# Kernel optimization log

Hardware: AMD Instinct MI355X
Metric: run time of the kernel (lower is better)

The kernel has to match this reference:

```python
import jax, jax.numpy as jnp
import numpy as np
import math

B, L, D, H, DK, DFF = 4, 1024, 1024, 16, 64, 4096
NUM_BUCKETS, MAX_DIST = 32, 128


def _relative_position_bucket(rel):
    # bidirectional T5 bucketing; rel = memory_pos - context_pos
    nb = NUM_BUCKETS // 2
    n = -rel
    ret = (n < 0).astype(jnp.int32) * nb
    n = jnp.abs(n)
    max_exact = nb // 2
    is_small = n < max_exact
    val_if_large = max_exact + (
        jnp.log(jnp.maximum(n, 1).astype(jnp.float32) / max_exact)
        / math.log(MAX_DIST / max_exact)
        * (nb - max_exact)
    ).astype(jnp.int32)
    val_if_large = jnp.minimum(val_if_large, nb - 1)
    return ret + jnp.where(is_small, n.astype(jnp.int32), val_if_large)


def t5_layernorm(x, w, eps):
    # no mean subtraction, no bias (T5 style)
    var = jnp.mean(jnp.square(x.astype(jnp.float32)), axis=-1, keepdims=True)
    return w * (x / jnp.sqrt(var + eps))


def setup_inputs() -> dict:
    key = jax.random.key(0)
    ks = jax.random.split(key, 12)
    inp = {
        "src": jax.random.normal(ks[0], (B, L, D), dtype=jnp.float32),
        "enc_position": jnp.broadcast_to(jnp.arange(L, dtype=jnp.int32), (B, L)),
        "ln1_w": jnp.ones((D,), jnp.float32),
        "wq": jax.random.normal(ks[1], (H * DK, D), jnp.float32) * (D * DK) ** -0.5,
        "bq": jnp.zeros((H * DK,), jnp.float32),
        "wk": jax.random.normal(ks[2], (H * DK, D), jnp.float32) * D ** -0.5,
        "bk": jnp.zeros((H * DK,), jnp.float32),
        "wv": jax.random.normal(ks[3], (H * DK, D), jnp.float32) * D ** -0.5,
        "bv": jnp.zeros((H * DK,), jnp.float32),
        "fc_w": jax.random.normal(ks[4], (D, H * DK), jnp.float32) * (H * DK) ** -0.5,
        "fc_b": jnp.zeros((D,), jnp.float32),
        "rel_bias": jax.random.normal(ks[5], (NUM_BUCKETS, H), jnp.float32) * 0.02,
        "ln2_w": jnp.ones((D,), jnp.float32),
        "wi": jax.random.normal(ks[6], (DFF, D), jnp.float32) * D ** -0.5,
        "wo": jax.random.normal(ks[7], (D, DFF), jnp.float32) * DFF ** -0.5,
    }
    return inp


def reference(src, enc_position, ln1_w, wq, bq, wk, bk, wv, bv, fc_w, fc_b,
              rel_bias, ln2_w, wi, wo):
    b, l, d = src.shape
    temp = DK ** 0.5

    # --- Multi-head self attention (pre-LN, T5 relative bias) ---
    proj = t5_layernorm(src, ln1_w, 1e-12)
    q = (proj @ wq.T + bq).reshape(b, l, H, DK).transpose(0, 2, 1, 3)  # [b,h,l,dk]
    k = (proj @ wk.T + bk).reshape(b, l, H, DK).transpose(0, 2, 1, 3)
    v = (proj @ wv.T + bv).reshape(b, l, H, DK).transpose(0, 2, 1, 3)

    # relative position bias: [b, h, l_q, l_k]
    rel = enc_position[:, None, :] - enc_position[:, :, None]  # mem - ctx
    bucket = _relative_position_bucket(rel)                    # [b, l, l]
    position_bias = rel_bias[bucket].transpose(0, 3, 1, 2)     # [b, h, l, l]

    scores = jnp.einsum("bhqd,bhkd->bhqk", q / temp, k) + position_bias
    attn = jax.nn.softmax(scores, axis=-1)                     # dropout = eval no-op
    ctx = jnp.einsum("bhqk,bhkd->bhqd", attn, v)
    ctx = ctx.transpose(0, 2, 1, 3).reshape(b, l, H * DK)
    attn_out = ctx @ fc_w.T + fc_b + src                       # residual
    attn_sum = jnp.sum(attn, axis=1)                           # [b, l, l]

    # --- Position-wise FFN (pre-LN, gelu, no biases) ---
    nx = t5_layernorm(attn_out, ln2_w, 1e-6)
    h = jax.nn.gelu(nx @ wi.T, approximate=False)
    out = attn_out + h @ wo.T
    return out, attn_sum, position_bias
```

## Files before the change

### kernel.cpp

```cpp
#include <hip/hip_runtime.h>
#include <hip/hip_bf16.h>
#include <math.h>

typedef __attribute__((ext_vector_type(8))) short short8;
typedef __attribute__((ext_vector_type(4))) float f32x4;
typedef unsigned short u16;

#define L2E 1.44269504088896340736f

__device__ __forceinline__ u16 f2bf(float f) {
  union { float f; unsigned u; } x; x.f = f;
  unsigned r = x.u + 0x7fffu + ((x.u >> 16) & 1u);
  return (u16)(r >> 16);
}

__device__ __forceinline__ void gload16(const void* g, void* l) {
  auto gp = reinterpret_cast<const __attribute__((address_space(1))) void*>(
      reinterpret_cast<uintptr_t>(g));
  auto lp = reinterpret_cast<__attribute__((address_space(3))) void*>(
      reinterpret_cast<uintptr_t>(l));
  __builtin_amdgcn_global_load_lds(gp, lp, 16, 0, 0);
}

__device__ __forceinline__ int xcd_swz(int flat, int nwg) {
  return (flat & 7) * (nwg >> 3) + (flat >> 3);
}

__device__ __forceinline__ int bucket_fn(int rel) {
  int n = -rel;
  int ret = 0;
  if (n < 0) { ret = 16; n = -n; }
  if (n < 8) return ret + n;
  int e = 31 - __clz(n);
  unsigned nn = (unsigned)n * (unsigned)n;
  int f = 2 * e + ((nn >= (1u << (2 * e + 1))) ? 1 : 0) - 6;
  int val = 8 + f;
  if (val > 15) val = 15;
  return ret + val;
}

__global__ __launch_bounds__(256) void prep_ln(
    const float* __restrict__ wq, const float* __restrict__ wk,
    const float* __restrict__ wv, const float* __restrict__ fcw,
    const float* __restrict__ wi, const float* __restrict__ wo,
    const float* __restrict__ bq, const float* __restrict__ bk,
    const float* __restrict__ bv, const float* __restrict__ rel_bias,
    u16* __restrict__ wqb, u16* __restrict__ wkb, u16* __restrict__ wvb,
    u16* __restrict__ fcwb, u16* __restrict__ wib, u16* __restrict__ wob,
    float* __restrict__ fb, float* __restrict__ tab,
    const float* __restrict__ src, const float* __restrict__ ln1_w,
    u16* __restrict__ proj) {
  const int blk = blockIdx.x, t = threadIdx.x;
  if (blk < 12288) {
    const float* s; u16* d; int rel;
    if (blk < 1024)      { s = wq;  d = wqb;  rel = blk; }
    else if (blk < 2048) { s = wk;  d = wkb;  rel = blk - 1024; }
    else if (blk < 3072) { s = wv;  d = wvb;  rel = blk - 2048; }
    else if (blk < 4096) { s = fcw; d = fcwb; rel = blk - 3072; }
    else if (blk < 8192) { s = wi;  d = wib;  rel = blk - 4096; }
    else                 { s = wo;  d = wob;  rel = blk - 8192; }
    const int i = (rel * 256 + t) * 4;
    float4 v = *(const float4*)&s[i];
    d[i + 0] = f2bf(v.x); d[i + 1] = f2bf(v.y);
    d[i + 2] = f2bf(v.z); d[i + 3] = f2bf(v.w);
  } else if (blk < 12300) {
    const int i = (blk - 12288) * 256 + t;
    fb[i] = i < 1024 ? bq[i] : (i < 2048 ? bk[i - 1024] : bv[i - 2048]);
  } else if (blk < 12428) {
    const int idx = (blk - 12300) * 256 + t;
    const int h = idx >> 11;
    const int rel = (idx & 2047) - 1024;
    tab[idx] = rel_bias[bucket_fn(rel) * 16 + h];
  } else {
    const int row = blk - 12428;
    const float4 v = ((const float4*)(src + (size_t)row * 1024))[t];
    float ss = v.x * v.x + v.y * v.y + v.z * v.z + v.w * v.w;
#pragma unroll
    for (int off = 1; off < 64; off <<= 1) ss += __shfl_xor(ss, off, 64);
    __shared__ float red[4];
    if ((t & 63) == 0) red[t >> 6] = ss;
    __syncthreads();
    float tot = red[0] + red[1] + red[2] + red[3];
    float inv = 1.0f / sqrtf(tot * (1.0f / 1024.0f) + 1e-12f);
    const float4 wv = ((const float4*)ln1_w)[t];
    u16* o = proj + (size_t)row * 1024 + t * 4;
    o[0] = f2bf(v.x * inv * wv.x);
    o[1] = f2bf(v.y * inv * wv.y);
    o[2] = f2bf(v.z * inv * wv.z);
    o[3] = f2bf(v.w * inv * wv.w);
  }
}

__global__ __launch_bounds__(256) void t5_ln(const float* __restrict__ x,
                                             const float* __restrict__ wgt,
                                             float eps, u16* __restrict__ out) {
  const int row = blockIdx.x, t = threadIdx.x;
  const float4 v = ((const float4*)(x + (size_t)row * 1024))[t];
  float ss = v.x * v.x + v.y * v.y + v.z * v.z + v.w * v.w;
#pragma unroll
  for (int off = 1; off < 64; off <<= 1) ss += __shfl_xor(ss, off, 64);
  __shared__ float red[4];
  if ((t & 63) == 0) red[t >> 6] = ss;
  __syncthreads();
  float tot = red[0] + red[1] + red[2] + red[3];
  float inv = 1.0f / sqrtf(tot * (1.0f / 1024.0f) + eps);
  const float4 wv = ((const float4*)wgt)[t];
  u16* o = out + (size_t)row * 1024 + t * 4;
  o[0] = f2bf(v.x * inv * wv.x);
  o[1] = f2bf(v.y * inv * wv.y);
  o[2] = f2bf(v.z * inv * wv.z);
  o[3] = f2bf(v.w * inv * wv.w);
}

__global__ __launch_bounds__(256) void transpose_v(const u16* __restrict__ v,
                                                   u16* __restrict__ vt) {
  __shared__ u16 T[64][72];
  const int bh = blockIdx.y;
  const int l0 = blockIdx.x * 64;
  const int t = threadIdx.x;
  const int sr = t >> 3, sc = (t & 7) * 8;
  const u16* vb = v + (size_t)bh * 65536;
  *(short8*)&T[sr][sc]      = *(const short8*)&vb[(size_t)(l0 + sr) * 64 + sc];
  *(short8*)&T[sr + 32][sc] = *(const short8*)&vb[(size_t)(l0 + sr + 32) * 64 + sc];
  __syncthreads();
  u16* vtb = vt + (size_t)bh * 65536;
  short8 o0, o1;
#pragma unroll
  for (int u = 0; u < 8; u++) {
    ((u16*)&o0)[u] = T[sc + u][sr];
    ((u16*)&o1)[u] = T[sc + u][sr + 32];
  }
  *(short8*)&vtb[(size_t)sr * 1024 + l0 + sc]        = o0;
  *(short8*)&vtb[(size_t)(sr + 32) * 1024 + l0 + sc] = o1;
}

template<int MODE>
__global__ __launch_bounds__(256, 3) void gemm_nt(
    const u16* __restrict__ A, const u16* __restrict__ Bw,
    int M, int N, int K,
    const float* __restrict__ bias, const float* __restrict__ res,
    float scale, float* __restrict__ outF, u16* __restrict__ outB) {
  __shared__ u16 As[3][4096];
  __shared__ u16 Bs[3][4096];
  const int t = threadIdx.x;
  const int w = t >> 6, lane = t & 63;
  const int wr = w >> 1, wc = w & 1;
  const int g = lane >> 4, lc = lane & 15;

  const int nwg = gridDim.x * gridDim.y;
  const int flat = xcd_swz(blockIdx.y * gridDim.x + blockIdx.x, nwg);
  const int bx = flat % gridDim.x, by = flat / gridDim.x;
  const int m0 = by * 128, n0 = bx * 128;

  const int srow = w * 16 + (lane >> 2);
  const int sc8  = (lane & 3) ^ ((srow >> 1) & 3);
  const u16* Ag = &A[(size_t)(m0 + srow) * K + sc8 * 8];
  const u16* Bg = &Bw[(size_t)(n0 + srow) * K + sc8 * 8];
  const size_t row64 = (size_t)64 * K;
  const int swz = (lc >> 1) & 3;

  const int NT = K >> 5;
  f32x4 acc[4][4] = {};

  auto stage = [&](int buf, int tt) {
    const int k0 = tt << 5;
    u16* lA = &As[buf][w * 512];
    u16* lB = &Bs[buf][w * 512];
    gload16(Ag + k0, lA);
    gload16(Ag + row64 + k0, lA + 2048);
    gload16(Bg + k0, lB);
    gload16(Bg + row64 + k0, lB + 2048);
  };

  stage(0, 0);
  stage(1, 1);

  for (int tt = 0; tt < NT; tt++) {
    const int cur = tt % 3;
    if (tt < NT - 1) {
      asm volatile("s_waitcnt vmcnt(4)" ::: "memory");
    } else {
      asm volatile("s_waitcnt vmcnt(0)" ::: "memory");
    }
    __builtin_amdgcn_s_barrier();
    if (tt + 2 < NT) stage((tt + 2) % 3, tt + 2);
    short8 af[4], bf[4];
#pragma unroll
    for (int mi = 0; mi < 4; mi++)
      af[mi] = *(short8*)&As[cur][(wr * 64 + mi * 16 + lc) * 32 + (g ^ swz) * 8];
#pragma unroll
    for (int ni = 0; ni < 4; ni++)
      bf[ni] = *(short8*)&Bs[cur][(wc * 64 + ni * 16 + lc) * 32 + (g ^ swz) * 8];
#pragma unroll
    for (int mi = 0; mi < 4; mi++)
#pragma unroll
      for (int ni = 0; ni < 4; ni++)
        acc[mi][ni] = __builtin_amdgcn_mfma_f32_16x16x32_bf16(af[mi], bf[ni], acc[mi][ni], 0, 0, 0);
  }

  u16* Es = &As[0][0];
  __syncthreads();
#pragma unroll
  for (int mi = 0; mi < 4; mi++) {
#pragma unroll
    for (int ni = 0; ni < 4; ni++) {
#pragma unroll
      for (int r = 0; r < 4; r++) {
        const int col = n0 + wc * 64 + ni * 16 + lc;
        float v = acc[mi][ni][r];
        if (MODE == 0) {
          v = (v + bias[col]) * ((col >> 10) == 0 ? scale : 1.0f);
        } else {
          v = 0.5f * v * (1.0f + erff(v * 0.70710678118654752440f));
        }
        Es[wr * 2048 + (g * 4 + r) * 128 + wc * 64 + ni * 16 + lc] = f2bf(v);
      }
    }
    __syncthreads();
    {
      const int rr = t >> 3;
      const int wr2 = rr >> 4, r16 = rr & 15;
      const int cc = (t & 7) * 16;
      short8 o0 = *(short8*)&Es[wr2 * 2048 + r16 * 128 + cc];
      short8 o1 = *(short8*)&Es[wr2 * 2048 + r16 * 128 + cc + 8];
      const int row = m0 + wr2 * 64 + mi * 16 + r16;
      if (MODE == 0) {
        const int col0 = n0 + cc;
        const int which = col0 >> 10, c = col0 & 1023;
        const int hh = c >> 6, dk = c & 63;
        const int b = row >> 10, pos = row & 1023;
        u16* dst = outB + (size_t)which * 4194304 +
                   (((size_t)(b * 16 + hh)) * 1024 + pos) * 64 + dk;
        *(short8*)dst = o0;
        *(short8*)(dst + 8) = o1;
      } else {
        u16* dst = outB + (size_t)row * (size_t)N + n0 + cc;
        *(short8*)dst = o0;
        *(short8*)(dst + 8) = o1;
      }
    }
    __syncthreads();
  }
}

template<int MODE>
__global__ __launch_bounds__(256, 4) void gemm_nt64(
    const u16* __restrict__ A, const u16* __restrict__ Bw,
    int M, int N, int K,
    const float* __restrict__ bias, const float* __restrict__ res,
    float* __restrict__ outF) {
  __shared__ u16 As[3][2048];
  __shared__ u16 Bs[3][4096];
  const int t = threadIdx.x;
  const int w = t >> 6, lane = t & 63;
  const int wr = w >> 1, wc = w & 1;
  const int g = lane >> 4, lc = lane & 15;

  const int nwg = gridDim.x * gridDim.y;
  const int flat = xcd_swz(blockIdx.y * gridDim.x + blockIdx.x, nwg);
  const int bx = flat % gridDim.x, by = flat / gridDim.x;
  const int m0 = by * 64, n0 = bx * 128;

  const int srow = w * 16 + (lane >> 2);
  const int sc8  = (lane & 3) ^ ((srow >> 1) & 3);
  const u16* Ag = &A[(size_t)(m0 + srow) * K + sc8 * 8];
  const u16* Bg = &Bw[(size_t)(n0 + srow) * K + sc8 * 8];
  const size_t row64 = (size_t)64 * K;
  const int swz = (lc >> 1) & 3;

  const int NT = K >> 5;
  f32x4 acc[2][4] = {};

  auto stage = [&](int buf, int tt) {
    const int k0 = tt << 5;
    gload16(Ag + k0, &As[buf][w * 512]);
    gload16(Bg + k0, &Bs[buf][w * 512]);
    gload16(Bg + row64 + k0, &Bs[buf][w * 512 + 2048]);
  };

  stage(0, 0);
  stage(1, 1);

  for (int tt = 0; tt < NT; tt++) {
    const int cur = tt % 3;
    if (tt < NT - 1) {
      asm volatile("s_waitcnt vmcnt(3)" ::: "memory");
    } else {
      asm volatile("s_waitcnt vmcnt(0)" ::: "memory");
    }
    __builtin_amdgcn_s_barrier();
    if (tt + 2 < NT) stage((tt + 2) % 3, tt + 2);
    short8 af[2], bf[4];
#pragma unroll
    for (int mi = 0; mi < 2; mi++)
      af[mi] = *(short8*)&As[cur][(wr * 32 + mi * 16 + lc) * 32 + (g ^ swz) * 8];
#pragma unroll
    for (int ni = 0; ni < 4; ni++)
      bf[ni] = *(short8*)&Bs[cur][(wc * 64 + ni * 16 + lc) * 32 + (g ^ swz) * 8];
#pragma unroll
    for (int mi = 0; mi < 2; mi++)
#pragma unroll
      for (int ni = 0; ni < 4; ni++)
        acc[mi][ni] = __builtin_amdgcn_mfma_f32_16x16x32_bf16(af[mi], bf[ni], acc[mi][ni], 0, 0, 0);
  }

#pragma unroll
  for (int mi = 0; mi < 2; mi++) {
#pragma unroll
    for (int ni = 0; ni < 4; ni++) {
#pragma unroll
      for (int r = 0; r < 4; r++) {
        const int row = m0 + wr * 32 + mi * 16 + g * 4 + r;
        const int col = n0 + wc * 64 + ni * 16 + lc;
        float v = acc[mi][ni][r];
        if (MODE == 1) {
          v += bias[col] + res[(size_t)row * 1024 + col];
        } else {
          v += res[(size_t)row * 1024 + col];
        }
        outF[(size_t)row * 1024 + col] = v;
      }
    }
  }
}

__global__ __launch_bounds__(256, 3) void fc_asum(
    const u16* __restrict__ ctx, const u16* __restrict__ fcw,
    const float* __restrict__ fc_b, const float* __restrict__ src,
    float* __restrict__ attn_out,
    const u16* __restrict__ q, const u16* __restrict__ k,
    const float* __restrict__ tab, const float* __restrict__ ml,
    float* __restrict__ asum) {
  __shared__ char pool[36864];
  const int t = threadIdx.x;
  const int w = t >> 6, lane = t & 63;
  const int g = lane >> 4, lc = lane & 15;

  if (blockIdx.x < 512) {
    u16* As = (u16*)pool;
    u16* Bs = (u16*)(pool + 12288);
    const int wr = w >> 1, wc = w & 1;
    const int flat = xcd_swz(blockIdx.x, 512);
    const int bx = flat & 7, by = flat >> 3;
    const int m0 = by * 64, n0 = bx * 128;
    const int K = 1024;

    const int srow = w * 16 + (lane >> 2);
    const int sc8  = (lane & 3) ^ ((srow >> 1) & 3);
    const u16* Ag = &ctx[(size_t)(m0 + srow) * K + sc8 * 8];
    const u16* Bg = &fcw[(size_t)(n0 + srow) * K + sc8 * 8];
    const size_t row64 = (size_t)64 * K;
    const int swz = (lc >> 1) & 3;

    const int NT = K >> 5;
    f32x4 acc[2][4] = {};

    auto stage = [&](int buf, int tt) {
      const int k0 = tt << 5;
      gload16(Ag + k0, &As[buf * 2048 + w * 512]);
      gload16(Bg + k0, &Bs[buf * 4096 + w * 512]);
      gload16(Bg + row64 + k0, &Bs[buf * 4096 + w * 512 + 2048]);
    };

    stage(0, 0);
    stage(1, 1);

    for (int tt = 0; tt < NT; tt++) {
      const int cur = tt % 3;
      if (tt < NT - 1) {
        asm volatile("s_waitcnt vmcnt(3)" ::: "memory");
      } else {
        asm volatile("s_waitcnt vmcnt(0)" ::: "memory");
      }
      __builtin_amdgcn_s_barrier();
      if (tt + 2 < NT) stage((tt + 2) % 3, tt + 2);
      short8 af[2], bf[4];
#pragma unroll
      for (int mi = 0; mi < 2; mi++)
        af[mi] = *(short8*)&As[cur * 2048 + (wr * 32 + mi * 16 + lc) * 32 + (g ^ swz) * 8];
#pragma unroll
      for (int ni = 0; ni < 4; ni++)
        bf[ni] = *(short8*)&Bs[cur * 4096 + (wc * 64 + ni * 16 + lc) * 32 + (g ^ swz) * 8];
#pragma unroll
      for (int mi = 0; mi < 2; mi++)
#pragma unroll
        for (int ni = 0; ni < 4; ni++)
          acc[mi][ni] = __builtin_amdgcn_mfma_f32_16x16x32_bf16(af[mi], bf[ni], acc[mi][ni], 0, 0, 0);
    }

#pragma unroll
    for (int mi = 0; mi < 2; mi++) {
#pragma unroll
      for (int ni = 0; ni < 4; ni++) {
#pragma unroll
        for (int r = 0; r < 4; r++) {
          const int row = m0 + wr * 32 + mi * 16 + g * 4 + r;
          const int col = n0 + wc * 64 + ni * 16 + lc;
          float v = acc[mi][ni][r] + fc_b[col] + src[(size_t)row * 1024 + col];
          attn_out[(size_t)row * 1024 + col] = v;
        }
      }
    }
  } else {
    u16* Ks = (u16*)pool;
    float* tabs = (float*)(pool + 8192);
    const int flat = xcd_swz(blockIdx.x - 512, 1024);
    const int j0 = (flat % 16) * 64;
    const int i0 = ((flat / 16) % 16) * 64;
    const int b = flat / 256;
    const int sr = t >> 3;
    const int swc = ((t & 7) ^ (sr & 7)) * 8;
    const int sc = (t & 7) * 8;
    const int rx = lc & 7;

    f32x4 acc[4] = {};

    for (int h = 0; h < 16; h++) {
      const int bh = b * 16 + h;
      __syncthreads();
      const u16* kb = k + (size_t)bh * 65536;
      *(short8*)&Ks[sr * 64 + swc]        = *(const short8*)&kb[(size_t)(j0 + sr) * 64 + sc];
      *(short8*)&Ks[(sr + 32) * 64 + swc] = *(const short8*)&kb[(size_t)(j0 + sr + 32) * 64 + sc];
      if (t < 127) tabs[t] = tab[h * 2048 + (j0 - i0 - 63 + t) + 1024] * L2E;
      __syncthreads();
      const u16* qb = q + (size_t)bh * 65536;
      short8 aq0 = *(const short8*)&qb[(size_t)(i0 + w * 16 + lc) * 64 + g * 8];
      short8 aq1 = *(const short8*)&qb[(size_t)(i0 + w * 16 + lc) * 64 + 32 + g * 8];
      f32x4 s[4] = {};
#pragma unroll
      for (int ni = 0; ni < 4; ni++) {
        short8 b0 = *(short8*)&Ks[(ni * 16 + lc) * 64 + (g ^ rx) * 8];
        short8 b1 = *(short8*)&Ks[(ni * 16 + lc) * 64 + ((4 + g) ^ rx) * 8];
        s[ni] = __builtin_amdgcn_mfma_f32_16x16x32_bf16(aq0, b0, s[ni], 0, 0, 0);
        s[ni] = __builtin_amdgcn_mfma_f32_16x16x32_bf16(aq1, b1, s[ni], 0, 0, 0);
      }
      float mm[4], li[4];
#pragma unroll
      for (int r = 0; r < 4; r++) {
        const int i = i0 + w * 16 + g * 4 + r;
        mm[r] = ml[(size_t)bh * 1024 + i];
        li[r] = 1.0f / ml[65536 + (size_t)bh * 1024 + i];
      }
#pragma unroll
      for (int ni = 0; ni < 4; ni++)
#pragma unroll
        for (int r = 0; r < 4; r++) {
          float sv = s[ni][r] + tabs[ni * 16 + lc - w * 16 - g * 4 - r + 63];
          acc[ni][r] += __builtin_amdgcn_exp2f(sv - mm[r]) * li[r];
        }
    }
#pragma unroll
    for (int ni = 0; ni < 4; ni++)
#pragma unroll
      for (int r = 0; r < 4; r++) {
        const int i = i0 + w * 16 + g * 4 + r;
        asum[((size_t)b * 1024 + i) * 1024 + j0 + ni * 16 + lc] = acc[ni][r];
      }
  }
}

__global__ __launch_bounds__(256) void attn_kernel(
    const u16* __restrict__ q, const u16* __restrict__ k,
    const u16* __restrict__ vt, const float* __restrict__ tab,
    u16* __restrict__ ctx, float* __restrict__ ml, float* __restrict__ pb) {
  const int flat = xcd_swz(blockIdx.y * 16 + blockIdx.x, 1024);
  const int bh = flat / 16;
  const int i0 = (flat % 16) * 64;
  const int h = bh & 15, b = bh >> 4;
  const int t = threadIdx.x, w = t >> 6, lane = t & 63;
  const int g = lane >> 4, lc = lane & 15;
  const int sr = t >> 3;
  const int swc = ((t & 7) ^ (sr & 7)) * 8;
  const int sc = (t & 7) * 8;

  __shared__ u16 Ks[2][64][64];
  __shared__ u16 Vts[2][64][64];
  __shared__ u16 P[4][16][64];
  __shared__ float tabs[2048];

  const u16* qb  = q + (size_t)bh * 65536;
  const u16* kb  = k + (size_t)bh * 65536;
  const u16* vtb = vt + (size_t)bh * 65536;

  ((float4*)tabs)[t]       = ((const float4*)(tab + h * 2048))[t];
  ((float4*)tabs)[t + 256] = ((const float4*)(tab + h * 2048))[t + 256];

  const short8 aq0 = *(const short8*)&qb[(size_t)(i0 + w * 16 + lc) * 64 + g * 8];
  const short8 aq1 = *(const short8*)&qb[(size_t)(i0 + w * 16 + lc) * 64 + 32 + g * 8];

  {
    short8 ka = *(const short8*)&kb[(size_t)sr * 64 + sc];
    short8 kc = *(const short8*)&kb[(size_t)(sr + 32) * 64 + sc];
    short8 va = *(const short8*)&vtb[(size_t)sr * 1024 + sc];
    short8 vc = *(const short8*)&vtb[(size_t)(sr + 32) * 1024 + sc];
    *(short8*)&Ks[0][sr][swc]       = ka;
    *(short8*)&Ks[0][sr + 32][swc]  = kc;
    *(short8*)&Vts[0][sr][swc]      = va;
    *(short8*)&Vts[0][sr + 32][swc] = vc;
  }
  __syncthreads();

  const int rx = lc & 7;
  const int ibase = 1024 - i0 - (w * 16 + g * 4) + lc;
  float* pbrow = pb + (size_t)bh * 1048576 + (size_t)i0 * 1024 + t * 4;

  float m_r[4] = {-INFINITY, -INFINITY, -INFINITY, -INFINITY};
  float l_r[4] = {0.f, 0.f, 0.f, 0.f};
  f32x4 cacc[4] = {};

  for (int tt = 0; tt < 16; tt++) {
    const int buf = tt & 1;
    const int j0 = tt * 64;

    short8 nka, nkc, nva, nvc;
    if (tt < 15) {
      const int jn = j0 + 64;
      nka = *(const short8*)&kb[(size_t)(jn + sr) * 64 + sc];
      nkc = *(const short8*)&kb[(size_t)(jn + sr + 32) * 64 + sc];
      nva = *(const short8*)&vtb[(size_t)sr * 1024 + jn + sc];
      nvc = *(const short8*)&vtb[(size_t)(sr + 32) * 1024 + jn + sc];
    }

    f32x4 s[4] = {};
#pragma unroll
    for (int ni = 0; ni < 4; ni++) {
      short8 b0 = *(short8*)&Ks[buf][ni * 16 + lc][(g ^ rx) * 8];
      short8 b1 = *(short8*)&Ks[buf][ni * 16 + lc][((4 + g) ^ rx) * 8];
      s[ni] = __builtin_amdgcn_mfma_f32_16x16x32_bf16(aq0, b0, s[ni], 0, 0, 0);
      s[ni] = __builtin_amdgcn_mfma_f32_16x16x32_bf16(aq1, b1, s[ni], 0, 0, 0);
    }
#pragma unroll
    for (int ni = 0; ni < 4; ni++)
#pragma unroll
      for (int r = 0; r < 4; r++)
        s[ni][r] = fmaf(tabs[ibase + j0 + ni * 16 - r], L2E, s[ni][r]);

#pragma unroll
    for (int r = 0; r < 4; r++) {
      float tm = fmaxf(fmaxf(s[0][r], s[1][r]), fmaxf(s[2][r], s[3][r]));
#pragma unroll
      for (int off = 1; off < 16; off <<= 1) tm = fmaxf(tm, __shfl_xor(tm, off, 64));
      const float mn = fmaxf(m_r[r], tm);
      const float scl = __builtin_amdgcn_exp2f(m_r[r] - mn);
      float rs = 0.f;
#pragma unroll
      for (int ni = 0; ni < 4; ni++) {
        float p = __builtin_amdgcn_exp2f(s[ni][r] - mn);
        s[ni][r] = p;
        rs += p;
      }
#pragma unroll
      for (int off = 1; off < 16; off <<= 1) rs += __shfl_xor(rs, off, 64);
      l_r[r] = l_r[r] * scl + rs;
      m_r[r] = mn;
#pragma unroll
      for (int d = 0; d < 4; d++) cacc[d][r] *= scl;
    }

#pragma unroll
    for (int ni = 0; ni < 4; ni++)
#pragma unroll
      for (int r = 0; r < 4; r++) {
        const int prow = g * 4 + r;
        P[w][prow][(((ni * 2 + (lc >> 3)) ^ (prow & 7)) << 3) | (lc & 7)] = f2bf(s[ni][r]);
      }

    short8 ap0 = *(short8*)&P[w][lc][(g ^ rx) * 8];
    short8 ap1 = *(short8*)&P[w][lc][((4 + g) ^ rx) * 8];
#pragma unroll
    for (int d = 0; d < 4; d++) {
      short8 bv0 = *(short8*)&Vts[buf][d * 16 + lc][(g ^ rx) * 8];
      short8 bv1 = *(short8*)&Vts[buf][d * 16 + lc][((4 + g) ^ rx) * 8];
      cacc[d] = __builtin_amdgcn_mfma_f32_16x16x32_bf16(ap0, bv0, cacc[d], 0, 0, 0);
      cacc[d] = __builtin_amdgcn_mfma_f32_16x16x32_bf16(ap1, bv1, cacc[d], 0, 0, 0);
    }

    {
#pragma unroll
      for (int r4 = 0; r4 < 4; r4++) {
        const int il = tt * 4 + r4;
        const int base = t * 4 - (i0 + il) + 1024;
        float4 o;
        o.x = tabs[base + 0];
        o.y = tabs[base + 1];
        o.z = tabs[base + 2];
        o.w = tabs[base + 3];
        *(float4*)&pbrow[(size_t)il * 1024] = o;
      }
    }

    if (tt < 15) {
      *(short8*)&Ks[buf ^ 1][sr][swc]       = nka;
      *(short8*)&Ks[buf ^ 1][sr + 32][swc]  = nkc;
      *(short8*)&Vts[buf ^ 1][sr][swc]      = nva;
      *(short8*)&Vts[buf ^ 1][sr + 32][swc] = nvc;
    }
    __syncthreads();
  }

  float inv[4];
#pragma unroll
  for (int r = 0; r < 4; r++) inv[r] = 1.0f / l_r[r];
#pragma unroll
  for (int d = 0; d < 4; d++)
#pragma unroll
    for (int r = 0; r < 4; r++) {
      const int pos = i0 + w * 16 + g * 4 + r;
      ctx[((size_t)b * 1024 + pos) * 1024 + h * 64 + d * 16 + lc] = f2bf(cacc[d][r] * inv[r]);
    }
  if (lc == 0) {
#pragma unroll
    for (int r = 0; r < 4; r++) {
      const int i = i0 + w * 16 + g * 4 + r;
      ml[(size_t)bh * 1024 + i] = m_r[r];
      ml[65536 + (size_t)bh * 1024 + i] = l_r[r];
    }
  }
}

extern "C" void kernel_launch(void* const* d_in, const int* in_sizes, int n_in,
                              void* d_out, int out_size, void* d_ws, size_t ws_size,
                              hipStream_t stream) {
  const float* src      = (const float*)d_in[0];
  const float* ln1_w    = (const float*)d_in[2];
  const float* wq       = (const float*)d_in[3];
  const float* bq       = (const float*)d_in[4];
  const float* wk       = (const float*)d_in[5];
  const float* bk       = (const float*)d_in[6];
  const float* wv       = (const float*)d_in[7];
  const float* bv       = (const float*)d_in[8];
  const float* fc_w     = (const float*)d_in[9];
  const float* fc_b     = (const float*)d_in[10];
  const float* rel_bias = (const float*)d_in[11];
  const float* ln2_w    = (const float*)d_in[12];
  const float* wi       = (const float*)d_in[13];
  const float* wo       = (const float*)d_in[14];

  const size_t MB = 1u << 20;
  char* ws = (char*)d_ws;
  u16* wq_b   = (u16*)(ws + 0 * MB);
  u16* wk_b   = (u16*)(ws + 2 * MB);
  u16* wv_b   = (u16*)(ws + 4 * MB);
  u16* fcw_b  = (u16*)(ws + 6 * MB);
  u16* wi_b   = (u16*)(ws + 8 * MB);
  u16* wo_b   = (u16*)(ws + 16 * MB);
  u16* proj_b = (u16*)(ws + 24 * MB);
  u16* q_b    = (u16*)(ws + 32 * MB);
  u16* k_b    = (u16*)(ws + 40 * MB);
  u16* v_b    = (u16*)(ws + 48 * MB);
  u16* vt_b   = (u16*)(ws + 56 * MB);
  u16* h_b    = (u16*)(ws + 32 * MB);
  u16* ctx_b  = (u16*)(ws + 64 * MB);
  float* attn_out = (float*)(ws + 72 * MB);
  float* ml   = (float*)(ws + 88 * MB);
  float* tab  = (float*)(ws + 88 * MB + 512 * 1024);
  float* fb   = (float*)(ws + 90 * MB);

  float* outF = (float*)d_out;
  float* asum = outF + 4194304;
  float* pb   = outF + 8388608;

  prep_ln<<<16524, 256, 0, stream>>>(wq, wk, wv, fc_w, wi, wo, bq, bk, bv, rel_bias,
                                     wq_b, wk_b, wv_b, fcw_b, wi_b, wo_b, fb, tab,
                                     src, ln1_w, proj_b);

  gemm_nt<0><<<dim3(24, 32), 256, 0, stream>>>(proj_b, wq_b, 4096, 3072, 1024, fb, nullptr,
                                               0.125f * L2E, nullptr, q_b);

  transpose_v<<<dim3(16, 64), 256, 0, stream>>>(v_b, vt_b);
  attn_kernel<<<dim3(16, 64), 256, 0, stream>>>(q_b, k_b, vt_b, tab, ctx_b, ml, pb);

  fc_asum<<<1536, 256, 0, stream>>>(ctx_b, fcw_b, fc_b, src, attn_out,
                                    q_b, k_b, tab, ml, asum);

  t5_ln<<<4096, 256, 0, stream>>>(attn_out, ln2_w, 1e-6f, proj_b);

  gemm_nt<2><<<dim3(32, 32), 256, 0, stream>>>(proj_b, wi_b, 4096, 4096, 1024, nullptr, nullptr,
                                               1.0f, nullptr, h_b);
  gemm_nt64<3><<<dim3(8, 64), 256, 0, stream>>>(h_b, wo_b, 4096, 1024, 4096, nullptr, attn_out, outF);
}
```

Measured before the change: 322.8 us.

## Fuse second T5 layernorm into fc epilogue and FFN1 GEMM row scaling

Removes the standalone t5_ln kernel. The fc GEMM epilogue now writes the weight-scaled bf16 activations and per-column-tile partial sums of squares. The FFN1 GEMM sums the eight partials per row and applies the inverse RMS to its accumulator before GELU. This drops one launch and a full read and write pass over attn_out. The cost is extra epilogue stores and reductions, plus rounding to bf16 before normalisation, which slightly changes numerics.

After: 325.2 us. About the same (+0.7%).

```diff
diff --git a/kernel.cpp b/kernel.cpp
--- a/kernel.cpp
+++ b/kernel.cpp
@@ -91,27 +91,6 @@
   }
 }
 
-__global__ __launch_bounds__(256) void t5_ln(const float* __restrict__ x,
-                                             const float* __restrict__ wgt,
-                                             float eps, u16* __restrict__ out) {
-  const int row = blockIdx.x, t = threadIdx.x;
-  const float4 v = ((const float4*)(x + (size_t)row * 1024))[t];
-  float ss = v.x * v.x + v.y * v.y + v.z * v.z + v.w * v.w;
-#pragma unroll
-  for (int off = 1; off < 64; off <<= 1) ss += __shfl_xor(ss, off, 64);
-  __shared__ float red[4];
-  if ((t & 63) == 0) red[t >> 6] = ss;
-  __syncthreads();
-  float tot = red[0] + red[1] + red[2] + red[3];
-  float inv = 1.0f / sqrtf(tot * (1.0f / 1024.0f) + eps);
-  const float4 wv = ((const float4*)wgt)[t];
-  u16* o = out + (size_t)row * 1024 + t * 4;
-  o[0] = f2bf(v.x * inv * wv.x);
-  o[1] = f2bf(v.y * inv * wv.y);
-  o[2] = f2bf(v.z * inv * wv.z);
-  o[3] = f2bf(v.w * inv * wv.w);
-}
-
 __global__ __launch_bounds__(256) void transpose_v(const u16* __restrict__ v,
                                                    u16* __restrict__ vt) {
   __shared__ u16 T[64][72];
@@ -138,10 +117,11 @@
 __global__ __launch_bounds__(256, 3) void gemm_nt(
     const u16* __restrict__ A, const u16* __restrict__ Bw,
     int M, int N, int K,
-    const float* __restrict__ bias, const float* __restrict__ res,
-    float scale, float* __restrict__ outF, u16* __restrict__ outB) {
+    const float* __restrict__ bias, const float* __restrict__ partials,
+    float scale, u16* __restrict__ outB) {
   __shared__ u16 As[3][4096];
   __shared__ u16 Bs[3][4096];
+  __shared__ float invr[128];
   const int t = threadIdx.x;
   const int w = t >> 6, lane = t & 63;
   const int wr = w >> 1, wc = w & 1;
@@ -198,6 +178,15 @@
         acc[mi][ni] = __builtin_amdgcn_mfma_f32_16x16x32_bf16(af[mi], bf[ni], acc[mi][ni], 0, 0, 0);
   }
 
+  if (MODE == 2) {
+    if (t < 128) {
+      float s8 = 0.f;
+#pragma unroll
+      for (int p = 0; p < 8; p++) s8 += partials[p * 4096 + m0 + t];
+      invr[t] = 1.0f / sqrtf(s8 * (1.0f / 1024.0f) + 1e-6f);
+    }
+  }
+
   u16* Es = &As[0][0];
   __syncthreads();
 #pragma unroll
@@ -211,6 +200,7 @@
         if (MODE == 0) {
           v = (v + bias[col]) * ((col >> 10) == 0 ? scale : 1.0f);
         } else {
+          v *= invr[wr * 64 + mi * 16 + g * 4 + r];
           v = 0.5f * v * (1.0f + erff(v * 0.70710678118654752440f));
         }
         Es[wr * 2048 + (g * 4 + r) * 128 + wc * 64 + ni * 16 + lc] = f2bf(v);
@@ -243,12 +233,10 @@
   }
 }
 
-template<int MODE>
-__global__ __launch_bounds__(256, 4) void gemm_nt64(
+__global__ __launch_bounds__(256, 4) void gemm_ffn2(
     const u16* __restrict__ A, const u16* __restrict__ Bw,
     int M, int N, int K,
-    const float* __restrict__ bias, const float* __restrict__ res,
-    float* __restrict__ outF) {
+    const float* __restrict__ res, float* __restrict__ outF) {
   __shared__ u16 As[3][2048];
   __shared__ u16 Bs[3][4096];
   const int t = threadIdx.x;
@@ -312,12 +300,7 @@
       for (int r = 0; r < 4; r++) {
         const int row = m0 + wr * 32 + mi * 16 + g * 4 + r;
         const int col = n0 + wc * 64 + ni * 16 + lc;
-        float v = acc[mi][ni][r];
-        if (MODE == 1) {
-          v += bias[col] + res[(size_t)row * 1024 + col];
-        } else {
-          v += res[(size_t)row * 1024 + col];
-        }
+        float v = acc[mi][ni][r] + res[(size_t)row * 1024 + col];
         outF[(size_t)row * 1024 + col] = v;
       }
     }
@@ -330,7 +313,9 @@
     float* __restrict__ attn_out,
     const u16* __restrict__ q, const u16* __restrict__ k,
     const float* __restrict__ tab, const float* __restrict__ ml,
-    float* __restrict__ asum) {
+    float* __restrict__ asum,
+    const float* __restrict__ ln2_w, u16* __restrict__ nxw,
+    float* __restrict__ partials) {
   __shared__ char pool[36864];
   const int t = threadIdx.x;
   const int w = t >> 6, lane = t & 63;
@@ -339,6 +324,7 @@
   if (blockIdx.x < 512) {
     u16* As = (u16*)pool;
     u16* Bs = (u16*)(pool + 12288);
+    float* ssql = (float*)(pool + 28672);
     const int wr = w >> 1, wc = w & 1;
     const int flat = xcd_swz(blockIdx.x, 512);
     const int bx = flat & 7, by = flat >> 3;
@@ -388,6 +374,7 @@
           acc[mi][ni] = __builtin_amdgcn_mfma_f32_16x16x32_bf16(af[mi], bf[ni], acc[mi][ni], 0, 0, 0);
     }
 
+    float ssq[2][4] = {};
 #pragma unroll
     for (int mi = 0; mi < 2; mi++) {
 #pragma unroll
@@ -398,8 +385,35 @@
           const int col = n0 + wc * 64 + ni * 16 + lc;
           float v = acc[mi][ni][r] + fc_b[col] + src[(size_t)row * 1024 + col];
           attn_out[(size_t)row * 1024 + col] = v;
+          nxw[(size_t)row * 1024 + col] = f2bf(v * ln2_w[col]);
+          ssq[mi][r] += v * v;
         }
       }
+    }
+#pragma unroll
+    for (int mi = 0; mi < 2; mi++)
+#pragma unroll
+      for (int r = 0; r < 4; r++) {
+#pragma unroll
+        for (int off = 1; off < 16; off <<= 1)
+          ssq[mi][r] += __shfl_xor(ssq[mi][r], off, 64);
+      }
+    if (wc == 0 && lc == 0) {
+#pragma unroll
+      for (int mi = 0; mi < 2; mi++)
+#pragma unroll
+        for (int r = 0; r < 4; r++)
+          ssql[wr * 32 + mi * 16 + g * 4 + r] = ssq[mi][r];
+    }
+    __syncthreads();
+    if (wc == 1 && lc == 0) {
+#pragma unroll
+      for (int mi = 0; mi < 2; mi++)
+#pragma unroll
+        for (int r = 0; r < 4; r++) {
+          const int lr = wr * 32 + mi * 16 + g * 4 + r;
+          partials[bx * 4096 + m0 + lr] = ssql[lr] + ssq[mi][r];
+        }
     }
   } else {
     u16* Ks = (u16*)pool;
@@ -655,6 +669,7 @@
   float* ml   = (float*)(ws + 88 * MB);
   float* tab  = (float*)(ws + 88 * MB + 512 * 1024);
   float* fb   = (float*)(ws + 90 * MB);
+  float* partials = (float*)(ws + 91 * MB);
 
   float* outF = (float*)d_out;
   float* asum = outF + 4194304;
@@ -665,17 +680,16 @@
                                      src, ln1_w, proj_b);
 
   gemm_nt<0><<<dim3(24, 32), 256, 0, stream>>>(proj_b, wq_b, 4096, 3072, 1024, fb, nullptr,
-                                               0.125f * L2E, nullptr, q_b);
+                                               0.125f * L2E, q_b);
 
   transpose_v<<<dim3(16, 64), 256, 0, stream>>>(v_b, vt_b);
   attn_kernel<<<dim3(16, 64), 256, 0, stream>>>(q_b, k_b, vt_b, tab, ctx_b, ml, pb);
 
   fc_asum<<<1536, 256, 0, stream>>>(ctx_b, fcw_b, fc_b, src, attn_out,
-                                    q_b, k_b, tab, ml, asum);
-
-  t5_ln<<<4096, 256, 0, stream>>>(attn_out, ln2_w, 1e-6f, proj_b);
-
-  gemm_nt<2><<<dim3(32, 32), 256, 0, stream>>>(proj_b, wi_b, 4096, 4096, 1024, nullptr, nullptr,
-                                               1.0f, nullptr, h_b);
-  gemm_nt64<3><<<dim3(8, 64), 256, 0, stream>>>(h_b, wo_b, 4096, 1024, 4096, nullptr, attn_out, outF);
-}
+                                    q_b, k_b, tab, ml, asum,
+                                    ln2_w, proj_b, partials);
+
+  gemm_nt<2><<<dim3(32, 32), 256, 0, stream>>>(proj_b, wi_b, 4096, 4096, 1024, nullptr, partials,
+                                               1.0f, h_b);
+  gemm_ffn2<<<dim3(8, 64), 256, 0, stream>>>(h_b, wo_b, 4096, 1024, 4096, attn_out, outF);
+}
```
